# Optimization experiments

Measured on AMD Instinct MI355X. Metric: run time of the kernel, lower is better.

Reference implementation:

```python
import jax, jax.numpy as jnp
import numpy as np

N_AP, N_UE, D = 256, 1024, 64  # dimension = 64 in source

def setup_inputs() -> dict:
    key = jax.random.key(0)
    ks = jax.random.split(key, 9)
    s = 1.0 / np.sqrt(2 * D)
    return {
        "ap_hid": jax.random.normal(ks[0], (N_AP, D), jnp.float32),
        "ue_hid": jax.random.normal(ks[1], (N_UE, D), jnp.float32),
        "edge_hid": jax.random.normal(ks[2], (N_AP, N_UE, D), jnp.float32),
        "W1": jax.random.normal(ks[3], (2 * D, D), jnp.float32) * s,
        "b1": jnp.zeros((D,), jnp.float32),
        "W2": jax.random.normal(ks[4], (2 * D, D), jnp.float32) * s,
        "b2": jnp.zeros((D,), jnp.float32),
        "W3": jax.random.normal(ks[5], (2 * D, D), jnp.float32) * s,
        "b3": jnp.zeros((D,), jnp.float32),
    }

def reference(ap_hid, ue_hid, edge_hid, W1, b1, W2, b2, W3, b3):
    # edge_hid[a, u] is the feature of edge (AP a, UE u); eid is (a, u) itself.
    A, U, d = edge_hid.shape

    # reduce_func_ap: per-AP mailbox over all UE neighbors -> mlp1(cat(ap_hid, edge_hid))
    ap_in = jnp.concatenate(
        [jnp.broadcast_to(ap_hid[:, None, :], (A, U, d)), edge_hid], axis=-1)  # [A,U,2d]
    ap_res = jax.nn.relu(jnp.einsum('auk,kd->aud', ap_in, W1) + b1)            # [A,U,d]

    # reduce_func_ue: per-UE mailbox over all AP neighbors -> mlp2(cat(ue_hid, edge_hid))
    edge_ua = jnp.swapaxes(edge_hid, 0, 1)                                     # [U,A,d]
    ue_in = jnp.concatenate(
        [jnp.broadcast_to(ue_hid[:, None, :], (U, A, d)), edge_ua], axis=-1)   # [U,A,2d]
    ue_res = jax.nn.relu(jnp.einsum('uak,kd->uad', ue_in, W2) + b2)            # [U,A,d]

    # message_func_edge: for edge (a,u), sum src AP's ap_result excluding the
    # mailbox slot whose eid matches this edge, plus same for dst UE's ue_result.
    ap_sum = ap_res.sum(axis=1)   # [A,d]
    ue_sum = ue_res.sum(axis=1)   # [U,d]
    agg = (ap_sum[:, None, :] - ap_res) \
        + (ue_sum[None, :, :] - jnp.swapaxes(ue_res, 0, 1))                     # [A,U,d]

    new = jnp.einsum('auk,kd->aud', jnp.concatenate([edge_hid, agg], axis=-1), W3) + b3
    return new  # new edge 'hid' for both AP2UE and UE2AP, shape [A,U,d]
```

## Files before the change

kernel.cpp:

```cpp
#include <hip/hip_runtime.h>


#define A_N 256
#define U_N 1024

typedef short short8 __attribute__((ext_vector_type(8)));
typedef float f32x4 __attribute__((ext_vector_type(4)));

__device__ __forceinline__ unsigned short f2bf(float f) {
  unsigned int u = __float_as_uint(f);
  return (unsigned short)((u + 0x7FFFu + ((u >> 16) & 1u)) >> 16);
}

__device__ __forceinline__ f32x4 mfma16(short8 a, short8 b, f32x4 c) {
  return __builtin_amdgcn_mfma_f32_16x16x32_bf16(a, b, c, 0, 0, 0);
}

__device__ __forceinline__ void cvt16(const float4& e0, const float4& e1,
                                      const float4& e2, const float4& e3,
                                      short8& a0, short8& a1) {
  a0[0] = (short)f2bf(e0.x); a0[1] = (short)f2bf(e0.y);
  a0[2] = (short)f2bf(e0.z); a0[3] = (short)f2bf(e0.w);
  a0[4] = (short)f2bf(e1.x); a0[5] = (short)f2bf(e1.y);
  a0[6] = (short)f2bf(e1.z); a0[7] = (short)f2bf(e1.w);
  a1[0] = (short)f2bf(e2.x); a1[1] = (short)f2bf(e2.y);
  a1[2] = (short)f2bf(e2.z); a1[3] = (short)f2bf(e2.w);
  a1[4] = (short)f2bf(e3.x); a1[5] = (short)f2bf(e3.y);
  a1[6] = (short)f2bf(e3.z); a1[7] = (short)f2bf(e3.w);
}

__device__ __forceinline__ void rowmlp_row(const float* __restrict__ in,
                                           const float* __restrict__ W,
                                           const float* __restrict__ bias,
                                           float* __restrict__ out, int r, int lane) {
  float rv = in[r * 64 + lane];
  float acc = bias ? bias[lane] : 0.f;
#pragma unroll
  for (int k = 0; k < 64; k++) acc += __shfl(rv, k, 64) * W[k * 64 + lane];
  out[r * 64 + lane] = acc;
}

__global__ __launch_bounds__(256) void k_prep(
    const float* __restrict__ ap_hid, const float* __restrict__ ue_hid,
    const float* __restrict__ W1, const float* __restrict__ b1,
    const float* __restrict__ W2, const float* __restrict__ b2,
    const float* __restrict__ W3, unsigned short* __restrict__ Wt,
    float* __restrict__ c1, float* __restrict__ c2) {
  int bx = blockIdx.x, tid = threadIdx.x;
  if (bx < 64) {
    int idx = bx * 256 + tid;
    int r = idx >> 6, k = idx & 63;
    int sec = r >> 6, d = r & 63;
    float v;
    if (sec == 0)      v = W1[(64 + k) * 64 + d];
    else if (sec == 1) v = W2[(64 + k) * 64 + d];
    else if (sec == 2) v = W3[k * 64 + d];
    else               v = W3[(64 + k) * 64 + d];
    Wt[r * 64 + k] = f2bf(v);
  } else if (bx < 128) {
    int r = (bx - 64) * 4 + (tid >> 6);
    rowmlp_row(ap_hid, W1, b1, c1, r, tid & 63);
  } else {
    int r = (bx - 128) * 4 + (tid >> 6);
    rowmlp_row(ue_hid, W2, b2, c2, r, tid & 63);
  }
}

__global__ __launch_bounds__(256) void k_pass1(
    const float* __restrict__ edge, const unsigned short* __restrict__ Wt,
    const float* __restrict__ c1, const float* __restrict__ c2,
    float* __restrict__ ap_part, float* __restrict__ ue_part) {
  __shared__ float ap_l[4 * 64];
  int tid = threadIdx.x, lane = tid & 63, w = tid >> 6;
  int fr = lane & 15, fq = lane >> 4;
  int chunk = blockIdx.x >> 4;
  int panel = blockIdx.x & 15;
  int a0 = chunk * 4;
  int u0 = panel * 64;
  int urow = u0 + w * 16 + fr;
  const float* erow = edge + urow * 64 + fq * 8;

  ap_l[tid] = 0.f;
  __syncthreads();

  short8 bw[8][2];
#pragma unroll
  for (int nt = 0; nt < 8; nt++)
#pragma unroll
    for (int ks = 0; ks < 2; ks++)
      bw[nt][ks] = *(const short8*)(Wt + (nt * 16 + fr) * 64 + ks * 32 + fq * 8);

  float c2v[4][4];
#pragma unroll
  for (int j = 0; j < 4; j++)
#pragma unroll
    for (int i = 0; i < 4; i++)
      c2v[j][i] = c2[(u0 + w * 16 + fq * 4 + i) * 64 + j * 16 + fr];

  float ureg[4][4];
#pragma unroll
  for (int j = 0; j < 4; j++)
#pragma unroll
    for (int i = 0; i < 4; i++) ureg[j][i] = 0.f;

  const float* p0 = erow + a0 * 65536;
  float4 e0 = *(const float4*)(p0);
  float4 e1 = *(const float4*)(p0 + 4);
  float4 e2 = *(const float4*)(p0 + 32);
  float4 e3 = *(const float4*)(p0 + 36);
  float c1v[4];
#pragma unroll
  for (int j = 0; j < 4; j++) c1v[j] = c1[a0 * 64 + j * 16 + fr];

  for (int c = 0; c < 4; c++) {
    int a = a0 + c;
    float4 n0, n1, n2, n3;
    float nc1[4];
    if (c < 3) {
      const float* np = erow + (a + 1) * 65536;
      n0 = *(const float4*)(np);
      n1 = *(const float4*)(np + 4);
      n2 = *(const float4*)(np + 32);
      n3 = *(const float4*)(np + 36);
#pragma unroll
      for (int j = 0; j < 4; j++) nc1[j] = c1[(a + 1) * 64 + j * 16 + fr];
    }
    short8 af0, af1;
    cvt16(e0, e1, e2, e3, af0, af1);

#pragma unroll
    for (int j = 0; j < 4; j++) {
      f32x4 acc = {0.f, 0.f, 0.f, 0.f};
      acc = mfma16(af0, bw[j][0], acc);
      acc = mfma16(af1, bw[j][1], acc);
      float cv = c1v[j];
      float rs = fmaxf(acc[0] + cv, 0.f) + fmaxf(acc[1] + cv, 0.f) +
                 fmaxf(acc[2] + cv, 0.f) + fmaxf(acc[3] + cv, 0.f);
      rs += __shfl_xor(rs, 16, 64);
      rs += __shfl_xor(rs, 32, 64);
      if (lane < 16) atomicAdd(&ap_l[c * 64 + j * 16 + lane], rs);
    }
#pragma unroll
    for (int j = 0; j < 4; j++) {
      f32x4 acc = {0.f, 0.f, 0.f, 0.f};
      acc = mfma16(af0, bw[4 + j][0], acc);
      acc = mfma16(af1, bw[4 + j][1], acc);
#pragma unroll
      for (int i = 0; i < 4; i++)
        ureg[j][i] += fmaxf(acc[i] + c2v[j][i], 0.f);
    }
    if (c < 3) {
      e0 = n0; e1 = n1; e2 = n2; e3 = n3;
#pragma unroll
      for (int j = 0; j < 4; j++) c1v[j] = nc1[j];
    }
  }
#pragma unroll
  for (int j = 0; j < 4; j++)
#pragma unroll
    for (int i = 0; i < 4; i++)
      ue_part[(chunk * 1024 + u0 + w * 16 + fq * 4 + i) * 64 + j * 16 + fr] =
          ureg[j][i];
  __syncthreads();
  ap_part[(panel * 256 + a0 + w) * 64 + lane] = ap_l[tid];
}

__global__ __launch_bounds__(256) void k_mid(
    const float* __restrict__ ap_part, const float* __restrict__ ue_part,
    const float* __restrict__ W3, const float* __restrict__ b3,
    float* __restrict__ s3, float* __restrict__ s4) {
  int bx = blockIdx.x, tid = threadIdx.x, lane = tid & 63;
  const float* W3b = W3 + 4096;
  if (bx < 64) {
    int r = bx * 4 + (tid >> 6);
    float v = 0.f;
#pragma unroll
    for (int p = 0; p < 16; p++) v += ap_part[(p * 256 + r) * 64 + lane];
    float acc = 0.f;
#pragma unroll
    for (int k = 0; k < 64; k++) acc += __shfl(v, k, 64) * W3b[k * 64 + lane];
    s3[r * 64 + lane] = acc;
  } else {
    int r = (bx - 64) * 4 + (tid >> 6);
    float v = 0.f;
#pragma unroll
    for (int p = 0; p < 64; p++) v += ue_part[(p * 1024 + r) * 64 + lane];
    float acc = b3[lane];
#pragma unroll
    for (int k = 0; k < 64; k++) acc += __shfl(v, k, 64) * W3b[k * 64 + lane];
    s4[r * 64 + lane] = acc;
  }
}

__global__ __launch_bounds__(256) void k_pass2(
    const float* __restrict__ edge, const unsigned short* __restrict__ Wt,
    const float* __restrict__ c1, const float* __restrict__ c2,
    const float* __restrict__ s3, const float* __restrict__ s4,
    float* __restrict__ out) {
  __shared__ unsigned short W_lds[256 * 72];
  __shared__ unsigned short t_lds[64 * 72];
  int tid = threadIdx.x, lane = tid & 63, w = tid >> 6;
  int fr = lane & 15, fq = lane >> 4;
  int a = blockIdx.x >> 2;
  int ubase = (blockIdx.x & 3) * 256;

#pragma unroll
  for (int it = 0; it < 8; it++) {
    int r = it * 32 + (tid >> 3), seg = tid & 7;
    *(uint4*)&W_lds[r * 72 + seg * 8] = *(const uint4*)(Wt + r * 64 + seg * 8);
  }

  float c1v[4], s3v[4];
#pragma unroll
  for (int j = 0; j < 4; j++) {
    c1v[j] = c1[a * 64 + j * 16 + fr];
    s3v[j] = s3[a * 64 + j * 16 + fr];
  }

  const float* er0 = edge + (a * 1024 + ubase + w * 16 + fr) * 64 + fq * 8;
  float4 e0 = *(const float4*)(er0);
  float4 e1 = *(const float4*)(er0 + 4);
  float4 e2 = *(const float4*)(er0 + 32);
  float4 e3 = *(const float4*)(er0 + 36);
  float c2v[4][4], s4v[4][4];
#pragma unroll
  for (int j = 0; j < 4; j++)
#pragma unroll
    for (int i = 0; i < 4; i++) {
      int u = ubase + w * 16 + fq * 4 + i;
      c2v[j][i] = c2[u * 64 + j * 16 + fr];
      s4v[j][i] = s4[u * 64 + j * 16 + fr];
    }

  __syncthreads();

  for (int pnl = 0; pnl < 4; pnl++) {
    int upan = ubase + pnl * 64;
    float4 n0, n1, n2, n3;
    float c2n[4][4], s4n[4][4];
    if (pnl < 3) {
      const float* nr = edge + (a * 1024 + upan + 64 + w * 16 + fr) * 64 + fq * 8;
      n0 = *(const float4*)(nr);
      n1 = *(const float4*)(nr + 4);
      n2 = *(const float4*)(nr + 32);
      n3 = *(const float4*)(nr + 36);
#pragma unroll
      for (int j = 0; j < 4; j++)
#pragma unroll
        for (int i = 0; i < 4; i++) {
          int u = upan + 64 + w * 16 + fq * 4 + i;
          c2n[j][i] = c2[u * 64 + j * 16 + fr];
          s4n[j][i] = s4[u * 64 + j * 16 + fr];
        }
    }
    short8 af0, af1;
    cvt16(e0, e1, e2, e3, af0, af1);

    f32x4 accP3[4];
#pragma unroll
    for (int j = 0; j < 4; j++) {
      const unsigned short* wr = &W_lds[(j * 16 + fr) * 72 + fq * 8];
      short8 b10 = *(const short8*)(wr);
      short8 b11 = *(const short8*)(wr + 32);
      short8 b20 = *(const short8*)(wr + 64 * 72);
      short8 b21 = *(const short8*)(wr + 64 * 72 + 32);
      short8 b30 = *(const short8*)(wr + 128 * 72);
      short8 b31 = *(const short8*)(wr + 128 * 72 + 32);
      f32x4 a1 = {0.f, 0.f, 0.f, 0.f};
      a1 = mfma16(af0, b10, a1);
      a1 = mfma16(af1, b11, a1);
      f32x4 a2 = {0.f, 0.f, 0.f, 0.f};
      a2 = mfma16(af0, b20, a2);
      a2 = mfma16(af1, b21, a2);
      f32x4 p3 = {0.f, 0.f, 0.f, 0.f};
      p3 = mfma16(af0, b30, p3);
      p3 = mfma16(af1, b31, p3);
      accP3[j] = p3;
#pragma unroll
      for (int i = 0; i < 4; i++) {
        float tv = fmaxf(a1[i] + c1v[j], 0.f) + fmaxf(a2[i] + c2v[j][i], 0.f);
        t_lds[(w * 16 + fq * 4 + i) * 72 + j * 16 + fr] = f2bf(tv);
      }
    }
    short8 tf0 = *(const short8*)&t_lds[(w * 16 + fr) * 72 + fq * 8];
    short8 tf1 = *(const short8*)&t_lds[(w * 16 + fr) * 72 + 32 + fq * 8];
#pragma unroll
    for (int j = 0; j < 4; j++) {
      const unsigned short* wr = &W_lds[(192 + j * 16 + fr) * 72 + fq * 8];
      short8 b0 = *(const short8*)(wr);
      short8 b1 = *(const short8*)(wr + 32);
      f32x4 acc = {0.f, 0.f, 0.f, 0.f};
      acc = mfma16(tf0, b0, acc);
      acc = mfma16(tf1, b1, acc);
#pragma unroll
      for (int i = 0; i < 4; i++) {
        int u = upan + w * 16 + fq * 4 + i;
        out[(a * 1024 + u) * 64 + j * 16 + fr] =
            accP3[j][i] - acc[i] + s3v[j] + s4v[j][i];
      }
    }
    if (pnl < 3) {
      e0 = n0; e1 = n1; e2 = n2; e3 = n3;
#pragma unroll
      for (int j = 0; j < 4; j++)
#pragma unroll
        for (int i = 0; i < 4; i++) {
          c2v[j][i] = c2n[j][i];
          s4v[j][i] = s4n[j][i];
        }
    }
  }
}

extern "C" void kernel_launch(void* const* d_in, const int* in_sizes, int n_in,
                              void* d_out, int out_size, void* d_ws, size_t ws_size,
                              hipStream_t stream) {
  const float* ap_hid = (const float*)d_in[0];
  const float* ue_hid = (const float*)d_in[1];
  const float* edge   = (const float*)d_in[2];
  const float* W1     = (const float*)d_in[3];
  const float* b1     = (const float*)d_in[4];
  const float* W2     = (const float*)d_in[5];
  const float* b2     = (const float*)d_in[6];
  const float* W3     = (const float*)d_in[7];
  const float* b3     = (const float*)d_in[8];
  float* out = (float*)d_out;

  char* ws = (char*)d_ws;
  unsigned short* Wt = (unsigned short*)ws;
  float* c1      = (float*)(ws + 32768);
  float* c2      = (float*)(ws + 98304);
  float* s3      = (float*)(ws + 360448);
  float* s4      = (float*)(ws + 425984);
  float* ap_part = (float*)(ws + 688128);
  float* ue_part = (float*)(ws + 4882432);

  k_prep<<<384, 256, 0, stream>>>(ap_hid, ue_hid, W1, b1, W2, b2, W3, Wt, c1, c2);
  k_pass1<<<1024, 256, 0, stream>>>(edge, Wt, c1, c2, ap_part, ue_part);
  k_mid<<<320, 256, 0, stream>>>(ap_part, ue_part, W3, b3, s3, s4);
  k_pass2<<<1024, 256, 0, stream>>>(edge, Wt, c1, c2, s3, s4, out);
}
```

Before: 168.7 us.

## Split UE partial reduction across waves and keep W3 fragments in registers

In k_mid, the UE branch now gives each UE row its own block: four waves each sum 16 of the 64 partial panels, and the results are combined through shared memory. This raises the grid from 320 to 1088 blocks so the long serial reduction is spread across more threads. In k_pass2, the W3 weight fragments are loaded once from global memory into registers instead of being staged in LDS, which halves the W_lds footprint and removes repeated LDS reads inside the loop. The cost is higher register pressure in pass2, which may lower occupancy.

```diff
diff --git a/kernel.cpp b/kernel.cpp
--- a/kernel.cpp
+++ b/kernel.cpp
@@ -169,10 +169,11 @@
     const float* __restrict__ ap_part, const float* __restrict__ ue_part,
     const float* __restrict__ W3, const float* __restrict__ b3,
     float* __restrict__ s3, float* __restrict__ s4) {
-  int bx = blockIdx.x, tid = threadIdx.x, lane = tid & 63;
+  __shared__ float red[4][64];
+  int bx = blockIdx.x, tid = threadIdx.x, lane = tid & 63, w = tid >> 6;
   const float* W3b = W3 + 4096;
   if (bx < 64) {
-    int r = bx * 4 + (tid >> 6);
+    int r = bx * 4 + w;
     float v = 0.f;
 #pragma unroll
     for (int p = 0; p < 16; p++) v += ap_part[(p * 256 + r) * 64 + lane];
@@ -181,14 +182,20 @@
     for (int k = 0; k < 64; k++) acc += __shfl(v, k, 64) * W3b[k * 64 + lane];
     s3[r * 64 + lane] = acc;
   } else {
-    int r = (bx - 64) * 4 + (tid >> 6);
+    int r = bx - 64;
     float v = 0.f;
 #pragma unroll
-    for (int p = 0; p < 64; p++) v += ue_part[(p * 1024 + r) * 64 + lane];
-    float acc = b3[lane];
-#pragma unroll
-    for (int k = 0; k < 64; k++) acc += __shfl(v, k, 64) * W3b[k * 64 + lane];
-    s4[r * 64 + lane] = acc;
+    for (int q = 0; q < 16; q++)
+      v += ue_part[((w * 16 + q) * 1024 + r) * 64 + lane];
+    red[w][lane] = v;
+    __syncthreads();
+    if (w == 0) {
+      float vv = red[0][lane] + red[1][lane] + red[2][lane] + red[3][lane];
+      float acc = b3[lane];
+#pragma unroll
+      for (int k = 0; k < 64; k++) acc += __shfl(vv, k, 64) * W3b[k * 64 + lane];
+      s4[r * 64 + lane] = acc;
+    }
   }
 }
 
@@ -197,7 +204,7 @@
     const float* __restrict__ c1, const float* __restrict__ c2,
     const float* __restrict__ s3, const float* __restrict__ s4,
     float* __restrict__ out) {
-  __shared__ unsigned short W_lds[256 * 72];
+  __shared__ unsigned short W_lds[128 * 72];
   __shared__ unsigned short t_lds[64 * 72];
   int tid = threadIdx.x, lane = tid & 63, w = tid >> 6;
   int fr = lane & 15, fq = lane >> 4;
@@ -205,10 +212,19 @@
   int ubase = (blockIdx.x & 3) * 256;
 
 #pragma unroll
-  for (int it = 0; it < 8; it++) {
+  for (int it = 0; it < 4; it++) {
     int r = it * 32 + (tid >> 3), seg = tid & 7;
     *(uint4*)&W_lds[r * 72 + seg * 8] = *(const uint4*)(Wt + r * 64 + seg * 8);
   }
+
+  short8 w3t[4][2], w3b[4][2];
+#pragma unroll
+  for (int j = 0; j < 4; j++)
+#pragma unroll
+    for (int ks = 0; ks < 2; ks++) {
+      w3t[j][ks] = *(const short8*)(Wt + (128 + j * 16 + fr) * 64 + ks * 32 + fq * 8);
+      w3b[j][ks] = *(const short8*)(Wt + (192 + j * 16 + fr) * 64 + ks * 32 + fq * 8);
+    }
 
   float c1v[4], s3v[4];
 #pragma unroll
@@ -264,8 +280,6 @@
       short8 b11 = *(const short8*)(wr + 32);
       short8 b20 = *(const short8*)(wr + 64 * 72);
       short8 b21 = *(const short8*)(wr + 64 * 72 + 32);
-      short8 b30 = *(const short8*)(wr + 128 * 72);
-      short8 b31 = *(const short8*)(wr + 128 * 72 + 32);
       f32x4 a1 = {0.f, 0.f, 0.f, 0.f};
       a1 = mfma16(af0, b10, a1);
       a1 = mfma16(af1, b11, a1);
@@ -273,8 +287,8 @@
       a2 = mfma16(af0, b20, a2);
       a2 = mfma16(af1, b21, a2);
       f32x4 p3 = {0.f, 0.f, 0.f, 0.f};
-      p3 = mfma16(af0, b30, p3);
-      p3 = mfma16(af1, b31, p3);
+      p3 = mfma16(af0, w3t[j][0], p3);
+      p3 = mfma16(af1, w3t[j][1], p3);
       accP3[j] = p3;
 #pragma unroll
       for (int i = 0; i < 4; i++) {
@@ -286,12 +300,9 @@
     short8 tf1 = *(const short8*)&t_lds[(w * 16 + fr) * 72 + 32 + fq * 8];
 #pragma unroll
     for (int j = 0; j < 4; j++) {
-      const unsigned short* wr = &W_lds[(192 + j * 16 + fr) * 72 + fq * 8];
-      short8 b0 = *(const short8*)(wr);
-      short8 b1 = *(const short8*)(wr + 32);
       f32x4 acc = {0.f, 0.f, 0.f, 0.f};
-      acc = mfma16(tf0, b0, acc);
-      acc = mfma16(tf1, b1, acc);
+      acc = mfma16(tf0, w3b[j][0], acc);
+      acc = mfma16(tf1, w3b[j][1], acc);
 #pragma unroll
       for (int i = 0; i < 4; i++) {
         int u = upan + w * 16 + fq * 4 + i;
@@ -337,6 +348,6 @@
 
   k_prep<<<384, 256, 0, stream>>>(ap_hid, ue_hid, W1, b1, W2, b2, W3, Wt, c1, c2);
   k_pass1<<<1024, 256, 0, stream>>>(edge, Wt, c1, c2, ap_part, ue_part);
-  k_mid<<<320, 256, 0, stream>>>(ap_part, ue_part, W3, b3, s3, s4);
+  k_mid<<<1088, 256, 0, stream>>>(ap_part, ue_part, W3, b3, s3, s4);
   k_pass2<<<1024, 256, 0, stream>>>(edge, Wt, c1, c2, s3, s4, out);
 }
```

Measured after the change: 171.5 us. No clear change (+1.7%).

## Fuse four kernel stages into one cooperative persistent kernel with grid syncs

Applied to the files above, without the earlier changes.

Replaces the four separate launches (prep, pass1, mid, pass2) with one cooperative kernel of 512 blocks. Each block handles two work units per pass, and the stages are separated by grid.sync plus thread fences. The aim is to remove inter-kernel launch gaps and drain/fill bubbles. The trade-offs are grid-barrier cost, less parallelism (512 blocks and an occupancy hint of 2), and a fallback to the old launches if the cooperative launch fails.

```diff
diff --git a/kernel.cpp b/kernel.cpp
--- a/kernel.cpp
+++ b/kernel.cpp
@@ -1,4 +1,7 @@
 #include <hip/hip_runtime.h>
+#include <hip/hip_cooperative_groups.h>
+
+namespace cg = cooperative_groups;
 
 
 #define A_N 256
@@ -40,15 +43,16 @@
   out[r * 64 + lane] = acc;
 }
 
-__global__ __launch_bounds__(256) void k_prep(
-    const float* __restrict__ ap_hid, const float* __restrict__ ue_hid,
-    const float* __restrict__ W1, const float* __restrict__ b1,
-    const float* __restrict__ W2, const float* __restrict__ b2,
-    const float* __restrict__ W3, unsigned short* __restrict__ Wt,
-    float* __restrict__ c1, float* __restrict__ c2) {
-  int bx = blockIdx.x, tid = threadIdx.x;
-  if (bx < 64) {
-    int idx = bx * 256 + tid;
+
+__device__ __forceinline__ void dev_prep_unit(
+    int unit, int tid, const float* __restrict__ ap_hid,
+    const float* __restrict__ ue_hid, const float* __restrict__ W1,
+    const float* __restrict__ b1, const float* __restrict__ W2,
+    const float* __restrict__ b2, const float* __restrict__ W3,
+    unsigned short* __restrict__ Wt, float* __restrict__ c1,
+    float* __restrict__ c2) {
+  if (unit < 64) {
+    int idx = unit * 256 + tid;
     int r = idx >> 6, k = idx & 63;
     int sec = r >> 6, d = r & 63;
     float v;
@@ -57,38 +61,27 @@
     else if (sec == 2) v = W3[k * 64 + d];
     else               v = W3[(64 + k) * 64 + d];
     Wt[r * 64 + k] = f2bf(v);
-  } else if (bx < 128) {
-    int r = (bx - 64) * 4 + (tid >> 6);
-    rowmlp_row(ap_hid, W1, b1, c1, r, tid & 63);
+  } else if (unit < 128) {
+    rowmlp_row(ap_hid, W1, b1, c1, (unit - 64) * 4 + (tid >> 6), tid & 63);
   } else {
-    int r = (bx - 128) * 4 + (tid >> 6);
-    rowmlp_row(ue_hid, W2, b2, c2, r, tid & 63);
-  }
-}
-
-__global__ __launch_bounds__(256) void k_pass1(
-    const float* __restrict__ edge, const unsigned short* __restrict__ Wt,
-    const float* __restrict__ c1, const float* __restrict__ c2,
-    float* __restrict__ ap_part, float* __restrict__ ue_part) {
-  __shared__ float ap_l[4 * 64];
-  int tid = threadIdx.x, lane = tid & 63, w = tid >> 6;
+    rowmlp_row(ue_hid, W2, b2, c2, (unit - 128) * 4 + (tid >> 6), tid & 63);
+  }
+}
+
+__device__ __forceinline__ void dev_pass1_unit(
+    int unit, int tid, float* ap_l, const float* __restrict__ edge,
+    const short8 (&bw)[8][2], const float* __restrict__ c1,
+    const float* __restrict__ c2, float* __restrict__ ap_part,
+    float* __restrict__ ue_part) {
+  int lane = tid & 63, w = tid >> 6;
   int fr = lane & 15, fq = lane >> 4;
-  int chunk = blockIdx.x >> 4;
-  int panel = blockIdx.x & 15;
-  int a0 = chunk * 4;
-  int u0 = panel * 64;
+  int chunk = unit >> 4, panel = unit & 15;
+  int a0 = chunk * 4, u0 = panel * 64;
   int urow = u0 + w * 16 + fr;
   const float* erow = edge + urow * 64 + fq * 8;
 
   ap_l[tid] = 0.f;
   __syncthreads();
-
-  short8 bw[8][2];
-#pragma unroll
-  for (int nt = 0; nt < 8; nt++)
-#pragma unroll
-    for (int ks = 0; ks < 2; ks++)
-      bw[nt][ks] = *(const short8*)(Wt + (nt * 16 + fr) * 64 + ks * 32 + fq * 8);
 
   float c2v[4][4];
 #pragma unroll
@@ -165,14 +158,15 @@
   ap_part[(panel * 256 + a0 + w) * 64 + lane] = ap_l[tid];
 }
 
-__global__ __launch_bounds__(256) void k_mid(
-    const float* __restrict__ ap_part, const float* __restrict__ ue_part,
-    const float* __restrict__ W3, const float* __restrict__ b3,
-    float* __restrict__ s3, float* __restrict__ s4) {
-  int bx = blockIdx.x, tid = threadIdx.x, lane = tid & 63;
+__device__ __forceinline__ void dev_mid_unit(
+    int unit, int tid, const float* __restrict__ ap_part,
+    const float* __restrict__ ue_part, const float* __restrict__ W3,
+    const float* __restrict__ b3, float* __restrict__ s3,
+    float* __restrict__ s4) {
+  int lane = tid & 63, w = tid >> 6;
   const float* W3b = W3 + 4096;
-  if (bx < 64) {
-    int r = bx * 4 + (tid >> 6);
+  if (unit < 64) {
+    int r = unit * 4 + w;
     float v = 0.f;
 #pragma unroll
     for (int p = 0; p < 16; p++) v += ap_part[(p * 256 + r) * 64 + lane];
@@ -181,7 +175,7 @@
     for (int k = 0; k < 64; k++) acc += __shfl(v, k, 64) * W3b[k * 64 + lane];
     s3[r * 64 + lane] = acc;
   } else {
-    int r = (bx - 64) * 4 + (tid >> 6);
+    int r = (unit - 64) * 4 + w;
     float v = 0.f;
 #pragma unroll
     for (int p = 0; p < 64; p++) v += ue_part[(p * 1024 + r) * 64 + lane];
@@ -192,23 +186,25 @@
   }
 }
 
-__global__ __launch_bounds__(256) void k_pass2(
-    const float* __restrict__ edge, const unsigned short* __restrict__ Wt,
-    const float* __restrict__ c1, const float* __restrict__ c2,
-    const float* __restrict__ s3, const float* __restrict__ s4,
-    float* __restrict__ out) {
-  __shared__ unsigned short W_lds[256 * 72];
-  __shared__ unsigned short t_lds[64 * 72];
-  int tid = threadIdx.x, lane = tid & 63, w = tid >> 6;
-  int fr = lane & 15, fq = lane >> 4;
-  int a = blockIdx.x >> 2;
-  int ubase = (blockIdx.x & 3) * 256;
-
+__device__ __forceinline__ void stage_Wlds(unsigned short* W_lds,
+                                           const unsigned short* __restrict__ Wt,
+                                           int tid) {
 #pragma unroll
   for (int it = 0; it < 8; it++) {
     int r = it * 32 + (tid >> 3), seg = tid & 7;
     *(uint4*)&W_lds[r * 72 + seg * 8] = *(const uint4*)(Wt + r * 64 + seg * 8);
   }
+}
+
+__device__ __forceinline__ void dev_pass2_unit(
+    int unit, int tid, const unsigned short* W_lds, unsigned short* t_lds,
+    const float* __restrict__ edge, const float* __restrict__ c1,
+    const float* __restrict__ c2, const float* __restrict__ s3,
+    const float* __restrict__ s4, float* __restrict__ out) {
+  int lane = tid & 63, w = tid >> 6;
+  int fr = lane & 15, fq = lane >> 4;
+  int a = unit >> 2;
+  int ubase = (unit & 3) * 256;
 
   float c1v[4], s3v[4];
 #pragma unroll
@@ -231,8 +227,6 @@
       c2v[j][i] = c2[u * 64 + j * 16 + fr];
       s4v[j][i] = s4[u * 64 + j * 16 + fr];
     }
-
-  __syncthreads();
 
   for (int pnl = 0; pnl < 4; pnl++) {
     int upan = ubase + pnl * 64;
@@ -312,6 +306,103 @@
   }
 }
 
+
+__global__ __launch_bounds__(256) void k_prep(
+    const float* __restrict__ ap_hid, const float* __restrict__ ue_hid,
+    const float* __restrict__ W1, const float* __restrict__ b1,
+    const float* __restrict__ W2, const float* __restrict__ b2,
+    const float* __restrict__ W3, unsigned short* __restrict__ Wt,
+    float* __restrict__ c1, float* __restrict__ c2) {
+  dev_prep_unit(blockIdx.x, threadIdx.x, ap_hid, ue_hid, W1, b1, W2, b2, W3,
+                Wt, c1, c2);
+}
+
+__global__ __launch_bounds__(256) void k_pass1(
+    const float* __restrict__ edge, const unsigned short* __restrict__ Wt,
+    const float* __restrict__ c1, const float* __restrict__ c2,
+    float* __restrict__ ap_part, float* __restrict__ ue_part) {
+  __shared__ float ap_l[256];
+  int tid = threadIdx.x, lane = tid & 63;
+  int fr = lane & 15, fq = lane >> 4;
+  short8 bw[8][2];
+#pragma unroll
+  for (int nt = 0; nt < 8; nt++)
+#pragma unroll
+    for (int ks = 0; ks < 2; ks++)
+      bw[nt][ks] = *(const short8*)(Wt + (nt * 16 + fr) * 64 + ks * 32 + fq * 8);
+  dev_pass1_unit(blockIdx.x, tid, ap_l, edge, bw, c1, c2, ap_part, ue_part);
+}
+
+__global__ __launch_bounds__(256) void k_mid(
+    const float* __restrict__ ap_part, const float* __restrict__ ue_part,
+    const float* __restrict__ W3, const float* __restrict__ b3,
+    float* __restrict__ s3, float* __restrict__ s4) {
+  dev_mid_unit(blockIdx.x, threadIdx.x, ap_part, ue_part, W3, b3, s3, s4);
+}
+
+__global__ __launch_bounds__(256) void k_pass2(
+    const float* __restrict__ edge, const unsigned short* __restrict__ Wt,
+    const float* __restrict__ c1, const float* __restrict__ c2,
+    const float* __restrict__ s3, const float* __restrict__ s4,
+    float* __restrict__ out) {
+  __shared__ unsigned short W_lds[256 * 72];
+  __shared__ unsigned short t_lds[64 * 72];
+  stage_Wlds(W_lds, Wt, threadIdx.x);
+  __syncthreads();
+  dev_pass2_unit(blockIdx.x, threadIdx.x, W_lds, t_lds, edge, c1, c2, s3, s4,
+                 out);
+}
+
+
+__global__ __launch_bounds__(256, 2) void k_fused(
+    const float* __restrict__ edge, const float* __restrict__ ap_hid,
+    const float* __restrict__ ue_hid,
+    const float* __restrict__ W1, const float* __restrict__ b1,
+    const float* __restrict__ W2, const float* __restrict__ b2,
+    const float* __restrict__ W3, const float* __restrict__ b3,
+    unsigned short* __restrict__ Wt, float* __restrict__ c1,
+    float* __restrict__ c2, float* __restrict__ s3, float* __restrict__ s4,
+    float* __restrict__ ap_part, float* __restrict__ ue_part,
+    float* __restrict__ out) {
+  __shared__ unsigned short W_lds[256 * 72];
+  __shared__ unsigned short t_lds[64 * 72];
+  __shared__ float ap_l[256];
+  cg::grid_group grid = cg::this_grid();
+  int bx = blockIdx.x, tid = threadIdx.x, lane = tid & 63;
+  int fr = lane & 15, fq = lane >> 4;
+
+  if (bx < 384)
+    dev_prep_unit(bx, tid, ap_hid, ue_hid, W1, b1, W2, b2, W3, Wt, c1, c2);
+  __threadfence();
+  grid.sync();
+  __threadfence();
+
+  {
+    short8 bw[8][2];
+#pragma unroll
+    for (int nt = 0; nt < 8; nt++)
+#pragma unroll
+      for (int ks = 0; ks < 2; ks++)
+        bw[nt][ks] = *(const short8*)(Wt + (nt * 16 + fr) * 64 + ks * 32 + fq * 8);
+    dev_pass1_unit(bx, tid, ap_l, edge, bw, c1, c2, ap_part, ue_part);
+    __syncthreads();
+    dev_pass1_unit(bx + 512, tid, ap_l, edge, bw, c1, c2, ap_part, ue_part);
+  }
+  __threadfence();
+  grid.sync();
+  __threadfence();
+
+  if (bx < 320) dev_mid_unit(bx, tid, ap_part, ue_part, W3, b3, s3, s4);
+  __threadfence();
+  grid.sync();
+  __threadfence();
+
+  stage_Wlds(W_lds, Wt, tid);
+  __syncthreads();
+  dev_pass2_unit(bx, tid, W_lds, t_lds, edge, c1, c2, s3, s4, out);
+  dev_pass2_unit(bx + 512, tid, W_lds, t_lds, edge, c1, c2, s3, s4, out);
+}
+
 extern "C" void kernel_launch(void* const* d_in, const int* in_sizes, int n_in,
                               void* d_out, int out_size, void* d_ws, size_t ws_size,
                               hipStream_t stream) {
@@ -335,8 +426,19 @@
   float* ap_part = (float*)(ws + 688128);
   float* ue_part = (float*)(ws + 4882432);
 
-  k_prep<<<384, 256, 0, stream>>>(ap_hid, ue_hid, W1, b1, W2, b2, W3, Wt, c1, c2);
-  k_pass1<<<1024, 256, 0, stream>>>(edge, Wt, c1, c2, ap_part, ue_part);
-  k_mid<<<320, 256, 0, stream>>>(ap_part, ue_part, W3, b3, s3, s4);
-  k_pass2<<<1024, 256, 0, stream>>>(edge, Wt, c1, c2, s3, s4, out);
-}
+  void* args[] = {(void*)&edge, (void*)&ap_hid, (void*)&ue_hid,
+                  (void*)&W1, (void*)&b1, (void*)&W2, (void*)&b2,
+                  (void*)&W3, (void*)&b3, (void*)&Wt, (void*)&c1, (void*)&c2,
+                  (void*)&s3, (void*)&s4, (void*)&ap_part, (void*)&ue_part,
+                  (void*)&out};
+  hipError_t err = hipLaunchCooperativeKernel((const void*)k_fused, dim3(512),
+                                              dim3(256), args, 0, stream);
+  if (err != hipSuccess) {
+    (void)hipGetLastError();
+    k_prep<<<384, 256, 0, stream>>>(ap_hid, ue_hid, W1, b1, W2, b2, W3, Wt,
+                                    c1, c2);
+    k_pass1<<<1024, 256, 0, stream>>>(edge, Wt, c1, c2, ap_part, ue_part);
+    k_mid<<<320, 256, 0, stream>>>(ap_part, ue_part, W3, b3, s3, s4);
+    k_pass2<<<1024, 256, 0, stream>>>(edge, Wt, c1, c2, s3, s4, out);
+  }
+}
```

Result: slower. 629.5 us (+273.1%).
